# Performance work log

Measured on AMD Instinct MI355X. Metric: run time of the kernel, lower is better.

## Reference

```python
import jax, jax.numpy as jnp
import numpy as np

N_NODES = 100000
N_EDGES = 3200000
N_GRAPHS = 1000


def gcn_conv(x, row, col, norm, W, b, num_nodes):
    # x: [N, F_in] -> [N, F_out]; PyG GCNConv: linear, then normalized scatter-add
    h = x @ W                                   # [N, F_out]
    msg = norm[:, None] * h[row]                # gather from source nodes
    out = jax.ops.segment_sum(msg, col, num_segments=num_nodes)  # scatter to targets
    return out + b


def gcn_norm(edge_index, edge_weight, num_nodes):
    # add self-loops with weight 1.0 (PyG default, improved=False)
    loops = jnp.arange(num_nodes, dtype=edge_index.dtype)
    row = jnp.concatenate([edge_index[0], loops])
    col = jnp.concatenate([edge_index[1], loops])
    w = jnp.concatenate([edge_weight, jnp.ones(num_nodes, edge_weight.dtype)])
    deg = jax.ops.segment_sum(w, col, num_segments=num_nodes)
    dinv = jnp.where(deg > 0, jax.lax.rsqrt(jnp.maximum(deg, 1e-30)), 0.0)
    norm = dinv[row] * w * dinv[col]
    return row, col, norm


def setup_inputs() -> dict:
    key = jax.random.key(0)
    ks = jax.random.split(key, 8)
    x = jax.random.normal(ks[0], (N_NODES, 3), dtype=jnp.float32)
    edge_index = jax.random.randint(ks[1], (2, N_EDGES), 0, N_NODES, dtype=jnp.int64)
    edge_weight = jax.random.uniform(ks[2], (N_EDGES,), dtype=jnp.float32)
    batch = jnp.sort(jax.random.randint(ks[3], (N_NODES,), 0, N_GRAPHS, dtype=jnp.int64))
    W1 = jax.random.normal(ks[4], (3, 16), dtype=jnp.float32) * (1.0 / np.sqrt(3))
    b1 = jnp.zeros((16,), jnp.float32)
    W2 = jax.random.normal(ks[5], (16, 16), dtype=jnp.float32) * 0.25
    b2 = jnp.zeros((16,), jnp.float32)
    Wlin = jax.random.normal(ks[6], (16, 7), dtype=jnp.float32) * 0.25
    blin = jnp.zeros((7,), jnp.float32)
    return {"x": x, "edge_index": edge_index, "edge_weight": edge_weight,
            "batch": batch, "W1": W1, "b1": b1, "W2": W2, "b2": b2,
            "Wlin": Wlin, "blin": blin}


def reference(x, edge_index, edge_weight, batch, W1, b1, W2, b2, Wlin, blin):
    num_nodes = x.shape[0]
    row, col, norm = gcn_norm(edge_index, edge_weight, num_nodes)
    h = jax.nn.relu(gcn_conv(x, row, col, norm, W1, b1, num_nodes))
    h = jax.nn.relu(gcn_conv(h, row, col, norm, W2, b2, num_nodes))
    pooled = jax.ops.segment_sum(h, batch, num_segments=N_GRAPHS)  # [G, 16]
    return pooled @ Wlin + blin  # [G, 7]
```

## Files before the change

### kernel.cpp

```cpp
#include <hip/hip_runtime.h>


#define SH 6
#define RB 64
#define KMAX 2048
#define KST (KMAX + 1)
#define TPB 256
#define BCAP 4096
#define PT 1024
#define PB 256
#define NP 4
#define ETCAP 12800
#define GSPAN 16

typedef unsigned short ushort_t;
typedef unsigned char u8;
typedef unsigned long long u64;

__device__ __forceinline__ ushort_t f2bf(float v) {
    unsigned u = __float_as_uint(v);
    u += 0x7FFFu + ((u >> 16) & 1u);
    return (ushort_t)(u >> 16);
}

__device__ __forceinline__ unsigned quantw(float w) {
    unsigned wq = (unsigned)__float2int_rn(w * 32768.0f);
    return wq > 32767u ? 32767u : wq;
}

__global__ __launch_bounds__(PT)
void k_part(const int* __restrict__ row, const int* __restrict__ col,
            const float* __restrict__ ew, unsigned* __restrict__ bcnt,
            unsigned* __restrict__ done, unsigned* __restrict__ bst,
            unsigned* __restrict__ bof, uint2* __restrict__ brc,
            int E, int K, int tile, int KP) {
    __shared__ unsigned lh[KMAX];
    __shared__ unsigned cur[KMAX];
    __shared__ unsigned wt[PT / 64];
    __shared__ unsigned lastFlag;
    __shared__ unsigned lc[ETCAP];
    __shared__ unsigned lp[ETCAP];
    int tid = threadIdx.x, b = blockIdx.x;
    int e0 = min(b * tile, E), e1 = min(b * tile + tile, E);
    int cnt = e1 - e0;
    unsigned base = (unsigned)e0;
    bool staged = (cnt <= ETCAP);
    for (int i = tid; i < KMAX; i += PT) lh[i] = 0u;
    __syncthreads();
    if (staged) {
        for (int j = tid; j < cnt; j += PT) {
            int e = e0 + j;
            int c = col[e];
            lc[j] = (unsigned)c;
            lp[j] = (unsigned)row[e] | (quantw(ew[e]) << 17);
            atomicAdd(&lh[c >> SH], 1u);
        }
    } else {
        for (int e = e0 + tid; e < e1; e += PT) atomicAdd(&lh[col[e] >> SH], 1u);
    }
    __syncthreads();
    for (int i = tid; i < K; i += PT) {
        unsigned c = lh[i];
        if (c) atomicAdd(&bcnt[i], c);
    }
    __syncthreads();
    if (tid == 0) {
        __threadfence();
        lastFlag = (atomicAdd(done, 1u) == (unsigned)(gridDim.x - 1)) ? 1u : 0u;
    }
    __syncthreads();
    if (lastFlag) {
        int i0g = tid << 1;
        unsigned g0 = (i0g < K) ? atomicAdd(&bcnt[i0g], 0u) : 0u;
        unsigned g1 = (i0g + 1 < K) ? atomicAdd(&bcnt[i0g + 1], 0u) : 0u;
        unsigned ts = g0 + g1, v = ts;
#pragma unroll
        for (int o = 1; o < 64; o <<= 1) {
            unsigned u = __shfl_up(v, o, 64);
            if ((tid & 63) >= o) v += u;
        }
        if ((tid & 63) == 63) wt[tid >> 6] = v;
        __syncthreads();
        if (tid == 0) {
            unsigned acc = 0;
#pragma unroll
            for (int w = 0; w < PT / 64; w++) { unsigned t = wt[w]; wt[w] = acc; acc += t; }
        }
        __syncthreads();
        unsigned ex = wt[tid >> 6] + (v - ts);
        if (i0g < K) bst[i0g] = ex;
        if (i0g + 1 < K) bst[i0g + 1] = ex + g0;
        __syncthreads();
    }
    int i0 = tid << 1;
    unsigned a0 = lh[i0], a1 = lh[i0 + 1];
    unsigned ts = a0 + a1, v = ts;
#pragma unroll
    for (int o = 1; o < 64; o <<= 1) {
        unsigned u = __shfl_up(v, o, 64);
        if ((tid & 63) >= o) v += u;
    }
    if ((tid & 63) == 63) wt[tid >> 6] = v;
    __syncthreads();
    if (tid == 0) {
        unsigned acc = 0;
#pragma unroll
        for (int w = 0; w < PT / 64; w++) { unsigned t = wt[w]; wt[w] = acc; acc += t; }
    }
    __syncthreads();
    unsigned ex = wt[tid >> 6] + (v - ts);
    unsigned* bo = bof + (size_t)b * KST;
    cur[i0] = base + ex;          bo[i0] = base + ex;
    cur[i0 + 1] = base + ex + a0; bo[i0 + 1] = base + ex + a0;
    if (tid == PT - 1) bo[KMAX] = base + ex + ts;
    __syncthreads();
    for (int p = 0; p < NP; ++p) {
        int lo = p * KP, hi = min(lo + KP, K);
        if (staged) {
            for (int j = tid; j < cnt; j += PT) {
                unsigned c = lc[j];
                int bkt = (int)(c >> SH);
                if (bkt >= lo && bkt < hi) {
                    unsigned pos = atomicAdd(&cur[bkt], 1u);
                    brc[pos] = make_uint2(lp[j], c);
                }
            }
        } else {
            for (int e = e0 + tid; e < e1; e += PT) {
                int c = col[e];
                int bkt = c >> SH;
                if (bkt >= lo && bkt < hi) {
                    unsigned pos = atomicAdd(&cur[bkt], 1u);
                    brc[pos] = make_uint2((unsigned)row[e] | (quantw(ew[e]) << 17),
                                          (unsigned)c);
                }
            }
        }
        __syncthreads();
    }
}

__global__ __launch_bounds__(TPB)
void k_grp(const uint2* __restrict__ brc, const unsigned* __restrict__ bof,
           const unsigned* __restrict__ bst, const float* __restrict__ x,
           const float* __restrict__ W1, unsigned* __restrict__ srt,
           unsigned* __restrict__ cptr, float* __restrict__ dinv,
           unsigned* __restrict__ g1b, float* __restrict__ acc1,
           int N, int E, int K) {
    int orig = blockIdx.x;
    int q8 = K >> 3, r8 = K & 7;
    int xcd = orig & 7, idx = orig >> 3;
    int k = (xcd < r8 ? xcd * (q8 + 1) : r8 * (q8 + 1) + (xcd - r8) * q8) + idx;
    int node0 = k << SH;

    __shared__ unsigned ebuf[BCAP];
    __shared__ u8 cbuf[BCAP];
    __shared__ u8 seg[BCAP];
    __shared__ unsigned rsrc[PB];
    __shared__ unsigned roff[PB + 1];
    __shared__ unsigned wt4[TPB / 64];
    __shared__ unsigned cnt64[RB], st64[RB], dq[RB];
    __shared__ float dl[RB], lx[RB * 3], lw[48];
    int tid = threadIdx.x;
    unsigned s = bst[k];
    if (tid < RB) { cnt64[tid] = 0u; dq[tid] = 0u; }
    if (tid < 48) lw[tid] = W1[tid];
    int nn = min(RB, N - node0);
    for (int i = tid; i < nn * 3; i += TPB) lx[i] = x[(size_t)node0 * 3 + i];

    unsigned rl;
    {
        unsigned s0 = bof[(size_t)tid * KST + k];
        unsigned s1 = bof[(size_t)tid * KST + k + 1];
        rsrc[tid] = s0;
        rl = s1 - s0;
    }
    unsigned v = rl;
#pragma unroll
    for (int o = 1; o < 64; o <<= 1) {
        unsigned u = __shfl_up(v, o, 64);
        if ((tid & 63) >= o) v += u;
    }
    if ((tid & 63) == 63) wt4[tid >> 6] = v;
    __syncthreads();
    if (tid == 0) {
        unsigned acc = 0;
#pragma unroll
        for (int w = 0; w < TPB / 64; w++) { unsigned t = wt4[w]; wt4[w] = acc; acc += t; }
    }
    __syncthreads();
    unsigned ex = wt4[tid >> 6] + (v - rl);
    roff[tid] = ex;
    if (tid == PB - 1) roff[PB] = ex + rl;
    __syncthreads();
    unsigned c = roff[PB];

    bool fits = (c <= (unsigned)BCAP);
    if (fits) {
        for (unsigned j = ex; j < ex + rl; ++j) seg[j] = (u8)tid;
        __syncthreads();
        for (unsigned j = tid; j < c; j += TPB) {
            unsigned r = seg[j];
            unsigned src = rsrc[r] + (j - roff[r]);
            uint2 p = brc[src];
            unsigned cl = p.y & 63u;
            ebuf[j] = p.x; cbuf[j] = (u8)cl;
            atomicAdd(&cnt64[cl], 1u);
            atomicAdd(&dq[cl], p.x >> 17);
        }
        __syncthreads();
        if (tid == 0) {
            unsigned acc = 0;
            for (int i = 0; i < RB; i++) { st64[i] = acc; acc += cnt64[i]; cnt64[i] = 0u; }
        }
        __syncthreads();
        for (unsigned j = tid; j < c; j += TPB) {
            unsigned cl = cbuf[j];
            unsigned pos = st64[cl] + atomicAdd(&cnt64[cl], 1u);
            srt[s + pos] = ebuf[j];
        }
    } else {
#define MAP_SRC(j, srcv)                                                       \
        {                                                                      \
            int lo = 0, hi = PB - 1;                                           \
            _Pragma("unroll")                                                  \
            for (int it = 0; it < 8; ++it) {                                   \
                int mid = (lo + hi + 1) >> 1;                                  \
                if (roff[mid] <= (j)) lo = mid; else hi = mid - 1;             \
            }                                                                  \
            (srcv) = rsrc[lo] + ((j) - roff[lo]);                              \
        }
        for (unsigned j = tid; j < c; j += TPB) {
            unsigned src; MAP_SRC(j, src);
            uint2 p = brc[src];
            unsigned cl = p.y & 63u;
            atomicAdd(&cnt64[cl], 1u);
            atomicAdd(&dq[cl], p.x >> 17);
        }
        __syncthreads();
        if (tid == 0) {
            unsigned acc = 0;
            for (int i = 0; i < RB; i++) { st64[i] = acc; acc += cnt64[i]; cnt64[i] = 0u; }
        }
        __syncthreads();
        for (unsigned j = tid; j < c; j += TPB) {
            unsigned src; MAP_SRC(j, src);
            uint2 p = brc[src];
            unsigned cl = p.y & 63u;
            unsigned pos = st64[cl] + atomicAdd(&cnt64[cl], 1u);
            srt[s + pos] = p.x;
        }
#undef MAP_SRC
    }
    __syncthreads();
    if (tid < RB) {
        float d = rsqrtf(1.0f + (float)dq[tid] * (1.0f / 32768.0f));
        dl[tid] = d;
        if (tid < nn) {
            dinv[node0 + tid] = d;
            cptr[node0 + tid] = s + st64[tid];
        }
    }
    if (tid == 0 && node0 + nn == N) cptr[N] = (unsigned)E;
    __syncthreads();
    float* gtmp = (float*)ebuf;
    for (int idx2 = tid; idx2 < nn * 16; idx2 += TPB) {
        int n = idx2 >> 4, f = idx2 & 15;
        float vv = dl[n] * (lx[n * 3] * lw[f] + lx[n * 3 + 1] * lw[16 + f] +
                            lx[n * 3 + 2] * lw[32 + f]);
        acc1[(size_t)(node0 + n) * 16 + f] = vv;
        gtmp[idx2] = vv;
    }
    __syncthreads();
    for (int idx2 = tid; idx2 < nn * 8; idx2 += TPB) {
        int n = idx2 >> 3, qq = idx2 & 7;
        g1b[(size_t)(node0 + n) * 8 + qq] =
            (unsigned)f2bf(gtmp[n * 16 + 2 * qq]) |
            ((unsigned)f2bf(gtmp[n * 16 + 2 * qq + 1]) << 16);
    }
}

__global__ __launch_bounds__(TPB)
void k_csr1(const unsigned* __restrict__ srt, const unsigned* __restrict__ cptr,
            const uint2* __restrict__ gb2, const float* __restrict__ acc1,
            const float* __restrict__ dinv, const float* __restrict__ b1,
            const float* __restrict__ W2, unsigned* __restrict__ g2b,
            float* __restrict__ acc2, int N) {
    int t = blockIdx.x * TPB + threadIdx.x;
    int c = t >> 2, f4 = t & 3;
    if (c >= N) return;
    unsigned e = cptr[c], end = cptr[c + 1];
    float s0 = 0.0f, s1 = 0.0f, s2 = 0.0f, s3 = 0.0f;
#pragma unroll 4
    for (; e < end; ++e) {
        unsigned m = srt[e];
        float w = (float)(m >> 17) * (1.0f / 32768.0f);
        uint2 u = gb2[(size_t)(m & 0x1FFFFu) * 4 + f4];
        s0 = fmaf(w, __uint_as_float(u.x << 16), s0);
        s1 = fmaf(w, __uint_as_float(u.x & 0xFFFF0000u), s1);
        s2 = fmaf(w, __uint_as_float(u.y << 16), s2);
        s3 = fmaf(w, __uint_as_float(u.y & 0xFFFF0000u), s3);
    }
    float d = dinv[c];
    const float4 se = *(const float4*)&acc1[(size_t)c * 16 + 4 * f4];
    const float4 bb = *(const float4*)&b1[4 * f4];
    float h[4];
    h[0] = fmaxf(bb.x + d * (se.x + s0), 0.0f);
    h[1] = fmaxf(bb.y + d * (se.y + s1), 0.0f);
    h[2] = fmaxf(bb.z + d * (se.z + s2), 0.0f);
    h[3] = fmaxf(bb.w + d * (se.w + s3), 0.0f);
    int base = (threadIdx.x & 63) & ~3;
    float o0 = 0.0f, o1 = 0.0f, o2 = 0.0f, o3 = 0.0f;
#pragma unroll
    for (int kk = 0; kk < 16; ++kk) {
        float hk = __shfl(h[kk & 3], base + (kk >> 2), 64);
        const float4 wv = *(const float4*)&W2[kk * 16 + 4 * f4];
        o0 = fmaf(hk, wv.x, o0);
        o1 = fmaf(hk, wv.y, o1);
        o2 = fmaf(hk, wv.z, o2);
        o3 = fmaf(hk, wv.w, o3);
    }
    float r0 = d * o0, r1 = d * o1, r2 = d * o2, r3 = d * o3;
    *(float4*)&acc2[(size_t)c * 16 + 4 * f4] = make_float4(r0, r1, r2, r3);
    g2b[(size_t)c * 8 + 2 * f4]     = (unsigned)f2bf(r0) | ((unsigned)f2bf(r1) << 16);
    g2b[(size_t)c * 8 + 2 * f4 + 1] = (unsigned)f2bf(r2) | ((unsigned)f2bf(r3) << 16);
}

__global__ __launch_bounds__(TPB)
void k_csr2(const unsigned* __restrict__ srt, const unsigned* __restrict__ cptr,
            const uint2* __restrict__ gb2, const float* __restrict__ acc2,
            const float* __restrict__ dinv, const float* __restrict__ b2,
            const int* __restrict__ batch, float* __restrict__ pooled,
            int N, int G) {
    __shared__ float lacc[GSPAN * 16];
    __shared__ int lb[64];
    int tid = threadIdx.x;
    int t = blockIdx.x * TPB + tid;
    int c = t >> 2, f4 = t & 3;
    int c0 = blockIdx.x * 64;
    int ncols = min(64, N - c0);
    if (tid < ncols) lb[tid] = batch[c0 + tid];
    if (tid < GSPAN * 16) lacc[tid] = 0.0f;
    __syncthreads();
    int gmin = lb[0], gmax = lb[ncols - 1];
    bool fits = (gmax - gmin) < GSPAN;

    float h0 = 0.0f, h1 = 0.0f, h2 = 0.0f, h3 = 0.0f;
    if (c < N) {
        unsigned e = cptr[c], end = cptr[c + 1];
        float s0 = 0.0f, s1 = 0.0f, s2 = 0.0f, s3 = 0.0f;
#pragma unroll 4
        for (; e < end; ++e) {
            unsigned m = srt[e];
            float w = (float)(m >> 17) * (1.0f / 32768.0f);
            uint2 u = gb2[(size_t)(m & 0x1FFFFu) * 4 + f4];
            s0 = fmaf(w, __uint_as_float(u.x << 16), s0);
            s1 = fmaf(w, __uint_as_float(u.x & 0xFFFF0000u), s1);
            s2 = fmaf(w, __uint_as_float(u.y << 16), s2);
            s3 = fmaf(w, __uint_as_float(u.y & 0xFFFF0000u), s3);
        }
        float d = dinv[c];
        const float4 se = *(const float4*)&acc2[(size_t)c * 16 + 4 * f4];
        const float4 bb = *(const float4*)&b2[4 * f4];
        h0 = fmaxf(bb.x + d * (se.x + s0), 0.0f);
        h1 = fmaxf(bb.y + d * (se.y + s1), 0.0f);
        h2 = fmaxf(bb.z + d * (se.z + s2), 0.0f);
        h3 = fmaxf(bb.w + d * (se.w + s3), 0.0f);
        int g = lb[c - c0];
        if (fits) {
            int o = (g - gmin) * 16 + 4 * f4;
            atomicAdd(&lacc[o],     h0);
            atomicAdd(&lacc[o + 1], h1);
            atomicAdd(&lacc[o + 2], h2);
            atomicAdd(&lacc[o + 3], h3);
        } else {
            atomicAdd(&pooled[(size_t)g * 16 + 4 * f4],     h0);
            atomicAdd(&pooled[(size_t)g * 16 + 4 * f4 + 1], h1);
            atomicAdd(&pooled[(size_t)g * 16 + 4 * f4 + 2], h2);
            atomicAdd(&pooled[(size_t)g * 16 + 4 * f4 + 3], h3);
        }
    }
    if (fits) {
        __syncthreads();
        if (tid < GSPAN * 16) {
            int g = gmin + (tid >> 4);
            float v = lacc[tid];
            if (g < G && v != 0.0f) atomicAdd(&pooled[(size_t)g * 16 + (tid & 15)], v);
        }
    }
}

__global__ void k_final(const float* __restrict__ pooled, const float* __restrict__ Wlin,
                        const float* __restrict__ blin, float* __restrict__ out, int G) {
    int t = blockIdx.x * blockDim.x + threadIdx.x;
    int g = t / 7, j = t % 7;
    if (g >= G) return;
    float v = blin[j];
#pragma unroll
    for (int f = 0; f < 16; f++) v += pooled[g * 16 + f] * Wlin[f * 7 + j];
    out[g * 7 + j] = v;
}

static inline int cdiv_i(long long a, long long b) { return (int)((a + b - 1) / b); }

extern "C" void kernel_launch(void* const* d_in, const int* in_sizes, int n_in,
                              void* d_out, int out_size, void* d_ws, size_t ws_size,
                              hipStream_t stream) {
    const float* x     = (const float*)d_in[0];
    const int*   ei    = (const int*)d_in[1];
    const float* ew    = (const float*)d_in[2];
    const int*   batch = (const int*)d_in[3];
    const float* W1    = (const float*)d_in[4];
    const float* b1    = (const float*)d_in[5];
    const float* W2    = (const float*)d_in[6];
    const float* b2    = (const float*)d_in[7];
    const float* Wlin  = (const float*)d_in[8];
    const float* blin  = (const float*)d_in[9];
    float* out = (float*)d_out;

    const int N = in_sizes[0] / 3;
    const int E = in_sizes[2];
    const int G = out_size / 7;
    const int K = (N + RB - 1) >> SH;
    const int tile = cdiv_i(E, PB);
    const int KP = cdiv_i(K, NP);
    const int* row = ei;
    const int* col = ei + E;

    uint2*    brc    = (uint2*)d_ws;
    unsigned* srt    = (unsigned*)(brc + E);
    float*    dinv   = (float*)(srt + E);
    unsigned* g1b    = (unsigned*)(dinv + N);
    unsigned* g2b    = g1b + (size_t)N * 8;
    float*    acc1   = (float*)(g2b + (size_t)N * 8);
    float*    acc2   = acc1 + (size_t)N * 16;
    unsigned* cptr   = (unsigned*)(acc2 + (size_t)N * 16);
    unsigned* bst    = cptr + N + 1;
    unsigned* bof    = bst + KMAX;
    unsigned* bcnt   = bof + (size_t)PB * KST;
    unsigned* done   = bcnt + KMAX;
    float*    pooled = (float*)(done + 1);

    hipMemsetAsync(bcnt, 0, (KMAX + 1 + (size_t)G * 16) * sizeof(unsigned), stream);

    k_part<<<PB, PT, 0, stream>>>(row, col, ew, bcnt, done, bst, bof, brc,
                                  E, K, tile, KP);
    k_grp<<<K, TPB, 0, stream>>>(brc, bof, bst, x, W1, srt, cptr, dinv, g1b, acc1,
                                 N, E, K);

    k_csr1<<<cdiv_i((long long)N * 4, TPB), TPB, 0, stream>>>(
        srt, cptr, (const uint2*)g1b, acc1, dinv, b1, W2, g2b, acc2, N);

    k_csr2<<<cdiv_i((long long)N * 4, TPB), TPB, 0, stream>>>(
        srt, cptr, (const uint2*)g2b, acc2, dinv, b2, batch, pooled, N, G);

    k_final<<<cdiv_i((long long)G * 7, TPB), TPB, 0, stream>>>(pooled, Wlin, blin, out, G);
}
```

Baseline: 221.4 us.

## Fuse final linear into csr2, recompute layer-1 self term, simplify gather loop

The final pooled-to-output linear is folded into k_csr2, using a last-block-done counter so one fewer kernel is launched. The acc1 buffer is no longer written in k_grp; k_csr1 recomputes the self-loop term from x and W1, which saves a 6.4MB write and read. The k_grp gather drops the seg-map indirection and has each thread copy its own contiguous run serially, which can make loads less coalesced and the work uneven across threads. The CSR loop unroll goes from 4 to 8.

```diff
diff --git a/kernel.cpp b/kernel.cpp
--- a/kernel.cpp
+++ b/kernel.cpp
@@ -145,8 +145,7 @@
            const unsigned* __restrict__ bst, const float* __restrict__ x,
            const float* __restrict__ W1, unsigned* __restrict__ srt,
            unsigned* __restrict__ cptr, float* __restrict__ dinv,
-           unsigned* __restrict__ g1b, float* __restrict__ acc1,
-           int N, int E, int K) {
+           unsigned* __restrict__ g1b, int N, int E, int K) {
     int orig = blockIdx.x;
     int q8 = K >> 3, r8 = K & 7;
     int xcd = orig & 7, idx = orig >> 3;
@@ -155,7 +154,6 @@
 
     __shared__ unsigned ebuf[BCAP];
     __shared__ u8 cbuf[BCAP];
-    __shared__ u8 seg[BCAP];
     __shared__ unsigned rsrc[PB];
     __shared__ unsigned roff[PB + 1];
     __shared__ unsigned wt4[TPB / 64];
@@ -168,11 +166,11 @@
     int nn = min(RB, N - node0);
     for (int i = tid; i < nn * 3; i += TPB) lx[i] = x[(size_t)node0 * 3 + i];
 
-    unsigned rl;
+    unsigned s0r, rl;
     {
         unsigned s0 = bof[(size_t)tid * KST + k];
         unsigned s1 = bof[(size_t)tid * KST + k + 1];
-        rsrc[tid] = s0;
+        rsrc[tid] = s0; s0r = s0;
         rl = s1 - s0;
     }
     unsigned v = rl;
@@ -197,14 +195,10 @@
 
     bool fits = (c <= (unsigned)BCAP);
     if (fits) {
-        for (unsigned j = ex; j < ex + rl; ++j) seg[j] = (u8)tid;
-        __syncthreads();
-        for (unsigned j = tid; j < c; j += TPB) {
-            unsigned r = seg[j];
-            unsigned src = rsrc[r] + (j - roff[r]);
-            uint2 p = brc[src];
+        for (unsigned j = 0; j < rl; ++j) {
+            uint2 p = brc[s0r + j];
             unsigned cl = p.y & 63u;
-            ebuf[j] = p.x; cbuf[j] = (u8)cl;
+            ebuf[ex + j] = p.x; cbuf[ex + j] = (u8)cl;
             atomicAdd(&cnt64[cl], 1u);
             atomicAdd(&dq[cl], p.x >> 17);
         }
@@ -268,7 +262,6 @@
         int n = idx2 >> 4, f = idx2 & 15;
         float vv = dl[n] * (lx[n * 3] * lw[f] + lx[n * 3 + 1] * lw[16 + f] +
                             lx[n * 3 + 2] * lw[32 + f]);
-        acc1[(size_t)(node0 + n) * 16 + f] = vv;
         gtmp[idx2] = vv;
     }
     __syncthreads();
@@ -282,16 +275,16 @@
 
 __global__ __launch_bounds__(TPB)
 void k_csr1(const unsigned* __restrict__ srt, const unsigned* __restrict__ cptr,
-            const uint2* __restrict__ gb2, const float* __restrict__ acc1,
-            const float* __restrict__ dinv, const float* __restrict__ b1,
-            const float* __restrict__ W2, unsigned* __restrict__ g2b,
-            float* __restrict__ acc2, int N) {
+            const uint2* __restrict__ gb2, const float* __restrict__ x,
+            const float* __restrict__ W1, const float* __restrict__ dinv,
+            const float* __restrict__ b1, const float* __restrict__ W2,
+            unsigned* __restrict__ g2b, float* __restrict__ acc2, int N) {
     int t = blockIdx.x * TPB + threadIdx.x;
     int c = t >> 2, f4 = t & 3;
     if (c >= N) return;
     unsigned e = cptr[c], end = cptr[c + 1];
     float s0 = 0.0f, s1 = 0.0f, s2 = 0.0f, s3 = 0.0f;
-#pragma unroll 4
+#pragma unroll 8
     for (; e < end; ++e) {
         unsigned m = srt[e];
         float w = (float)(m >> 17) * (1.0f / 32768.0f);
@@ -302,13 +295,20 @@
         s3 = fmaf(w, __uint_as_float(u.y & 0xFFFF0000u), s3);
     }
     float d = dinv[c];
-    const float4 se = *(const float4*)&acc1[(size_t)c * 16 + 4 * f4];
+    float xx0 = x[(size_t)c * 3], xx1 = x[(size_t)c * 3 + 1], xx2 = x[(size_t)c * 3 + 2];
+    const float4 w0 = *(const float4*)&W1[4 * f4];
+    const float4 w1 = *(const float4*)&W1[16 + 4 * f4];
+    const float4 w2 = *(const float4*)&W1[32 + 4 * f4];
+    float g0 = d * (xx0 * w0.x + xx1 * w1.x + xx2 * w2.x);
+    float g1 = d * (xx0 * w0.y + xx1 * w1.y + xx2 * w2.y);
+    float g2 = d * (xx0 * w0.z + xx1 * w1.z + xx2 * w2.z);
+    float g3 = d * (xx0 * w0.w + xx1 * w1.w + xx2 * w2.w);
     const float4 bb = *(const float4*)&b1[4 * f4];
     float h[4];
-    h[0] = fmaxf(bb.x + d * (se.x + s0), 0.0f);
-    h[1] = fmaxf(bb.y + d * (se.y + s1), 0.0f);
-    h[2] = fmaxf(bb.z + d * (se.z + s2), 0.0f);
-    h[3] = fmaxf(bb.w + d * (se.w + s3), 0.0f);
+    h[0] = fmaxf(bb.x + d * (g0 + s0), 0.0f);
+    h[1] = fmaxf(bb.y + d * (g1 + s1), 0.0f);
+    h[2] = fmaxf(bb.z + d * (g2 + s2), 0.0f);
+    h[3] = fmaxf(bb.w + d * (g3 + s3), 0.0f);
     int base = (threadIdx.x & 63) & ~3;
     float o0 = 0.0f, o1 = 0.0f, o2 = 0.0f, o3 = 0.0f;
 #pragma unroll
@@ -331,9 +331,12 @@
             const uint2* __restrict__ gb2, const float* __restrict__ acc2,
             const float* __restrict__ dinv, const float* __restrict__ b2,
             const int* __restrict__ batch, float* __restrict__ pooled,
+            unsigned* __restrict__ done2, const float* __restrict__ Wlin,
+            const float* __restrict__ blin, float* __restrict__ out,
             int N, int G) {
     __shared__ float lacc[GSPAN * 16];
     __shared__ int lb[64];
+    __shared__ unsigned lastFlag;
     int tid = threadIdx.x;
     int t = blockIdx.x * TPB + tid;
     int c = t >> 2, f4 = t & 3;
@@ -345,11 +348,10 @@
     int gmin = lb[0], gmax = lb[ncols - 1];
     bool fits = (gmax - gmin) < GSPAN;
 
-    float h0 = 0.0f, h1 = 0.0f, h2 = 0.0f, h3 = 0.0f;
     if (c < N) {
         unsigned e = cptr[c], end = cptr[c + 1];
         float s0 = 0.0f, s1 = 0.0f, s2 = 0.0f, s3 = 0.0f;
-#pragma unroll 4
+#pragma unroll 8
         for (; e < end; ++e) {
             unsigned m = srt[e];
             float w = (float)(m >> 17) * (1.0f / 32768.0f);
@@ -362,10 +364,10 @@
         float d = dinv[c];
         const float4 se = *(const float4*)&acc2[(size_t)c * 16 + 4 * f4];
         const float4 bb = *(const float4*)&b2[4 * f4];
-        h0 = fmaxf(bb.x + d * (se.x + s0), 0.0f);
-        h1 = fmaxf(bb.y + d * (se.y + s1), 0.0f);
-        h2 = fmaxf(bb.z + d * (se.z + s2), 0.0f);
-        h3 = fmaxf(bb.w + d * (se.w + s3), 0.0f);
+        float h0 = fmaxf(bb.x + d * (se.x + s0), 0.0f);
+        float h1 = fmaxf(bb.y + d * (se.y + s1), 0.0f);
+        float h2 = fmaxf(bb.z + d * (se.z + s2), 0.0f);
+        float h3 = fmaxf(bb.w + d * (se.w + s3), 0.0f);
         int g = lb[c - c0];
         if (fits) {
             int o = (g - gmin) * 16 + 4 * f4;
@@ -388,17 +390,28 @@
             if (g < G && v != 0.0f) atomicAdd(&pooled[(size_t)g * 16 + (tid & 15)], v);
         }
     }
-}
-
-__global__ void k_final(const float* __restrict__ pooled, const float* __restrict__ Wlin,
-                        const float* __restrict__ blin, float* __restrict__ out, int G) {
-    int t = blockIdx.x * blockDim.x + threadIdx.x;
-    int g = t / 7, j = t % 7;
-    if (g >= G) return;
-    float v = blin[j];
-#pragma unroll
-    for (int f = 0; f < 16; f++) v += pooled[g * 16 + f] * Wlin[f * 7 + j];
-    out[g * 7 + j] = v;
+    __syncthreads();
+    if (tid == 0) {
+        __threadfence();
+        lastFlag = (atomicAdd(done2, 1u) == (unsigned)(gridDim.x - 1)) ? 1u : 0u;
+    }
+    __syncthreads();
+    if (lastFlag) {
+        __threadfence();
+        for (int g = tid; g < G; g += TPB) {
+            float p[16];
+#pragma unroll
+            for (int f = 0; f < 16; f++)
+                p[f] = atomicAdd(&pooled[(size_t)g * 16 + f], 0.0f);
+#pragma unroll
+            for (int j = 0; j < 7; j++) {
+                float v = blin[j];
+#pragma unroll
+                for (int f = 0; f < 16; f++) v = fmaf(p[f], Wlin[f * 7 + j], v);
+                out[(size_t)g * 7 + j] = v;
+            }
+        }
+    }
 }
 
 static inline int cdiv_i(long long a, long long b) { return (int)((a + b - 1) / b); }
@@ -432,27 +445,26 @@
     float*    dinv   = (float*)(srt + E);
     unsigned* g1b    = (unsigned*)(dinv + N);
     unsigned* g2b    = g1b + (size_t)N * 8;
-    float*    acc1   = (float*)(g2b + (size_t)N * 8);
-    float*    acc2   = acc1 + (size_t)N * 16;
+    float*    acc2   = (float*)(g2b + (size_t)N * 8);
     unsigned* cptr   = (unsigned*)(acc2 + (size_t)N * 16);
     unsigned* bst    = cptr + N + 1;
     unsigned* bof    = bst + KMAX;
     unsigned* bcnt   = bof + (size_t)PB * KST;
     unsigned* done   = bcnt + KMAX;
-    float*    pooled = (float*)(done + 1);
-
-    hipMemsetAsync(bcnt, 0, (KMAX + 1 + (size_t)G * 16) * sizeof(unsigned), stream);
+    unsigned* done2  = done + 1;
+    float*    pooled = (float*)(done2 + 1);
+
+    hipMemsetAsync(bcnt, 0, (KMAX + 2 + (size_t)G * 16) * sizeof(unsigned), stream);
 
     k_part<<<PB, PT, 0, stream>>>(row, col, ew, bcnt, done, bst, bof, brc,
                                   E, K, tile, KP);
-    k_grp<<<K, TPB, 0, stream>>>(brc, bof, bst, x, W1, srt, cptr, dinv, g1b, acc1,
+    k_grp<<<K, TPB, 0, stream>>>(brc, bof, bst, x, W1, srt, cptr, dinv, g1b,
                                  N, E, K);
 
     k_csr1<<<cdiv_i((long long)N * 4, TPB), TPB, 0, stream>>>(
-        srt, cptr, (const uint2*)g1b, acc1, dinv, b1, W2, g2b, acc2, N);
+        srt, cptr, (const uint2*)g1b, x, W1, dinv, b1, W2, g2b, acc2, N);
 
     k_csr2<<<cdiv_i((long long)N * 4, TPB), TPB, 0, stream>>>(
-        srt, cptr, (const uint2*)g2b, acc2, dinv, b2, batch, pooled, N, G);
-
-    k_final<<<cdiv_i((long long)G * 7, TPB), TPB, 0, stream>>>(pooled, Wlin, blin, out, G);
-}
+        srt, cptr, (const uint2*)g2b, acc2, dinv, b2, batch, pooled,
+        done2, Wlin, blin, out, N, G);
+}
```

After: 281.9 us. +27.3%, slower.
